# Kernel optimization log

Hardware: AMD Instinct MI355X
Metric: run time of the kernel (lower is better)

## Reference

```python
import jax, jax.numpy as jnp
import numpy as np

# Module constants (match init_kwargs)
M = 2049                      # NpointsMesh (odd)
TAU = 2.821e-5                # Gaussian spreading width ~ 12*(pi/M)^2
XLIMS = (0.0, 10.0)
L = abs(XLIMS[1] - XLIMS[0])
KGRID = jnp.asarray(np.linspace(-(M // 2), M // 2, M), dtype=jnp.float32)        # (M,)
XGRID = jnp.asarray(2.0 * np.pi * np.linspace(XLIMS[0], XLIMS[1], M + 1)[:-1] / L,
                    dtype=jnp.float32)                                           # (M,)
FOUR_PI = 4.0 * np.pi


def setup_inputs() -> dict:
    key = jax.random.key(0)
    kx, = jax.random.split(key, 1)
    x = jax.random.uniform(kx, (16, 1024), dtype=jnp.float32) * 10.0  # points in [xLims[0], xLims[1])
    ones = jnp.ones((1,), dtype=jnp.float32)  # tf.initializers.ones for all 4 weights
    return {"x": x, "shift0": ones, "amp0": ones, "shift1": ones, "amp1": ones}


def reference(x, shift0, amp0, shift1, amp1):
    # Gaussian spreading: (B, N, M)
    diff = x[..., None] * (2.0 * np.pi / L) - XGRID
    g = jnp.exp(-jnp.square(diff) / (4.0 * TAU))
    # Sum over points -> gridded density (B, M), then FFT + shift
    gsum = jnp.sum(g, axis=1).astype(jnp.complex64)
    fft_g = jnp.fft.fftshift(jnp.fft.fft(gsum, axis=-1), axes=-1) * (L / (2.0 * np.pi))
    # Deconvolution of the Gaussian kernel (real-valued)
    deconv = jnp.sqrt(np.pi / TAU) * jnp.exp(jnp.square(KGRID) * TAU)  # (M,)
    rfft = fft_g * deconv  # (B, M) complex
    # Fourier multipliers (real; imag parts are structurally zero in the original)
    m1 = -amp0 * FOUR_PI / (jnp.square(KGRID) + jnp.square(5.0 * shift0))            # (M,)
    m2 = amp1 * FOUR_PI * jnp.square(1.0 / (jnp.square(KGRID) + jnp.square(5.0 * shift1)))  # (M,)
    mult = jnp.stack([m1, m2], axis=0)  # (2, M)
    mult_fft = mult[None, :, :].astype(jnp.complex64) * rfft[:, None, :]  # (B, 2, M)
    mult_deconv = mult_fft * deconv  # second deconv application, as in the original
    # Inverse FFT back to the mesh, keep real part: (B, 2, M)
    irfft = jnp.real(jnp.fft.ifft(jnp.fft.ifftshift(mult_deconv, axes=-1), axis=-1))
    # Inverse interpolation back to the points: (B, N, 2, M) -> (B, N, 2)
    local = irfft[:, None, :, :] * g[:, :, None, :]
    fmm = jnp.sum(local, axis=-1) / M
    return fmm
```

## Files before the change

kernel.cpp:

```cpp
#include <hip/hip_runtime.h>
#include <math.h>

#define M_   2049
#define B_   16
#define N_   1024
#define TAU_ 2.821e-5
#define PI_  3.14159265358979323846
#define TWO_PI_ 6.283185307179586476925286766559

#define CV_SPLIT 16
#define MPAD     2052

#define GS_CH    8
#define HT_BLKS  65
#define FMM_LPP  16

#define SW(i) ((i) + ((i) >> 2))

__global__ __launch_bounds__(256)
void spread_h4(const float* __restrict__ x,
               const float* __restrict__ s0, const float* __restrict__ a0,
               const float* __restrict__ s1, const float* __restrict__ a1,
               double* __restrict__ gsum_part, double* __restrict__ hhalf) {
    __shared__ double smem[4803];
    const int bx  = blockIdx.x;
    const int tid = threadIdx.x;

    if (bx < GS_CH * B_) {
        const int b  = bx >> 3;
        const int ch = bx & (GS_CH - 1);
        for (int i = tid; i < M_; i += 256) smem[i] = 0.0;
        __syncthreads();
        const int pl  = tid >> 1;
        const int sub = tid & 1;
        const double du      = TWO_PI_ / (double)M_;
        const double inv4tau = 1.0 / (4.0 * TAU_);
        const double xv = (double)x[(b << 10) + (ch << 7) + pl];
        const double u  = xv * (TWO_PI_ / 10.0);
        const int mc = (int)(xv * ((double)M_ / 10.0) + 0.5);
        const int start = mc - 33 + sub * 34;
        for (int i = 0; i < 34; ++i) {
            int m = start + i;
            if (m >= 0 && m < M_) {
                double d = u - du * (double)m;
                double t = d * d * inv4tau;
                if (t < 88.0) atomicAdd(&smem[m], (double)__expf(-(float)t));
            }
        }
        __syncthreads();
        double* gp = gsum_part + ((size_t)ch * B_ + b) * M_;
        for (int i = tid; i < M_; i += 256) gp[i] = smem[i];
    } else {
        const int dtile = bx - GS_CH * B_;
        double* costab = smem;
        double* cf0    = smem + 2049;
        double* cf1    = smem + 3073;
        double* red    = smem + 4097;
        double* cc     = smem + 4609;
        double* cs     = smem + 4642;
        double* fc     = smem + 4675;
        double* fs     = smem + 4739;
        const double th = TWO_PI_ / (double)M_;
        if (tid < 33) {
            double a = th * 64.0 * (double)tid;
            cc[tid] = cos(a);
            cs[tid] = sin(a);
        } else if (tid >= 64 && tid < 128) {
            double a = th * (double)(tid - 64);
            fc[tid - 64] = cos(a);
            fs[tid - 64] = sin(a);
        }
        const double sA = 5.0 * (double)s0[0], sB = 5.0 * (double)s1[0];
        const double amp0 = (double)a0[0],     amp1 = (double)a1[0];
        for (int jj = tid; jj < 1024; jj += 256) {
            double j  = (double)(jj + 1);
            double k2 = j * j;
            double dec2 = (PI_ / TAU_) * exp(2.0 * TAU_ * k2);
            double base = 2.0 * (10.0 / TWO_PI_) * dec2 / (double)M_;
            cf0[jj] = base * (-amp0 * 4.0 * PI_ / (k2 + sA * sA));
            double den = k2 + sB * sB;
            cf1[jj] = base * (amp1 * 4.0 * PI_ / (den * den));
        }
        __syncthreads();
        for (int i = tid; i < M_; i += 256) {
            int q = i >> 6, r = i & 63;
            costab[i] = cc[q] * fc[r] - cs[q] * fs[r];
        }
        __syncthreads();
        const int dl = tid & 15;
        const int jq = tid >> 4;
        const int d  = (dtile << 4) + dl;
        double acc0 = 0.0, acc1 = 0.0;
        if (d <= 1024) {
            const int jlo = (jq << 6) + 1;
            int r = (int)(((long long)jlo * (long long)d) % M_);
            #pragma unroll 4
            for (int jj = 0; jj < 64; ++jj) {
                double cv_ = costab[r];
                acc0 += cf0[(jq << 6) + jj] * cv_;
                acc1 += cf1[(jq << 6) + jj] * cv_;
                r += d; if (r >= M_) r -= M_;
            }
        }
        red[tid]       = acc0;
        red[256 + tid] = acc1;
        __syncthreads();
        if (tid < 16) {
            const int dd = (dtile << 4) + tid;
            if (dd <= 1024) {
                const double w0base = (10.0 / TWO_PI_) * (PI_ / TAU_) / (double)M_;
                double h0 = w0base * (-amp0 * 4.0 * PI_ / (sA * sA));
                double h1 = w0base * (amp1 * 4.0 * PI_ / ((sB * sB) * (sB * sB)));
                #pragma unroll
                for (int q = 0; q < 16; ++q) {
                    h0 += red[(q << 4) + tid];
                    h1 += red[256 + (q << 4) + tid];
                }
                hhalf[dd]        = h0;
                hhalf[1025 + dd] = h1;
            }
        }
    }
}

__global__ void conv_kernel(const double* __restrict__ gsum_part,
                            const double* __restrict__ hhalf,
                            double* __restrict__ part) {
    __shared__ double w0s[1456];
    __shared__ double w1s[1456];
    __shared__ double red[512];
    __shared__ double gls[132];
    const int mt = blockIdx.x;
    const int s  = blockIdx.y;
    const int b  = blockIdx.z;
    const int m0  = mt * 1024;
    const int p0  = (s * M_) / CV_SPLIT;
    const int p1  = ((s + 1) * M_) / CV_SPLIT;
    const int len = p1 - p0;
    const int wcount = 1024 + len;
    int base = m0 - (p0 + len - 1);
    while (base < 0) base += M_;
    for (int i = threadIdx.x; i < wcount; i += 256) {
        int idx = base + i;
        while (idx >= M_) idx -= M_;
        int dd = (idx > 1024) ? (M_ - idx) : idx;
        w0s[SW(i)] = hhalf[dd];
        w1s[SW(i)] = hhalf[1025 + dd];
    }
    for (int i = threadIdx.x; i < len; i += 256) {
        double acc = 0.0;
        #pragma unroll
        for (int ch = 0; ch < GS_CH; ++ch)
            acc += gsum_part[((size_t)ch * B_ + b) * M_ + p0 + i];
        gls[i] = acc;
    }
    __syncthreads();

    const int q = 4 * threadIdx.x + len - 1;
    double A0 = w0s[SW(q)], A1 = w0s[SW(q+1)], A2 = w0s[SW(q+2)], A3 = w0s[SW(q+3)];
    double C0 = w1s[SW(q)], C1 = w1s[SW(q+1)], C2 = w1s[SW(q+2)], C3 = w1s[SW(q+3)];
    double a00=0.0,a01=0.0,a02=0.0,a03=0.0, a10=0.0,a11=0.0,a12=0.0,a13=0.0;
    int j = q, tt = 0;
    for (; tt + 4 <= len; tt += 4) {
        double g;
        g = gls[tt];
        a00 += g*A0; a01 += g*A1; a02 += g*A2; a03 += g*A3;
        a10 += g*C0; a11 += g*C1; a12 += g*C2; a13 += g*C3;
        A3 = w0s[SW(j-1)]; C3 = w1s[SW(j-1)];
        g = gls[tt+1];
        a00 += g*A3; a01 += g*A0; a02 += g*A1; a03 += g*A2;
        a10 += g*C3; a11 += g*C0; a12 += g*C1; a13 += g*C2;
        A2 = w0s[SW(j-2)]; C2 = w1s[SW(j-2)];
        g = gls[tt+2];
        a00 += g*A2; a01 += g*A3; a02 += g*A0; a03 += g*A1;
        a10 += g*C2; a11 += g*C3; a12 += g*C0; a13 += g*C1;
        A1 = w0s[SW(j-3)]; C1 = w1s[SW(j-3)];
        g = gls[tt+3];
        a00 += g*A1; a01 += g*A2; a02 += g*A3; a03 += g*A0;
        a10 += g*C1; a11 += g*C2; a12 += g*C3; a13 += g*C0;
        A0 = w0s[SW(j-4)]; C0 = w1s[SW(j-4)];
        j -= 4;
    }
    for (; tt < len; ++tt) {
        double g = gls[tt];
        a00 += g*A0; a01 += g*A1; a02 += g*A2; a03 += g*A3;
        a10 += g*C0; a11 += g*C1; a12 += g*C2; a13 += g*C3;
    }
    {
        double* pv = part + (((size_t)s * B_ + b) * 2) * MPAD + m0 + 4 * threadIdx.x;
        pv[0]        = a00; pv[1]        = a01; pv[2]        = a02; pv[3]        = a03;
        pv[MPAD + 0] = a10; pv[MPAD + 1] = a11; pv[MPAD + 2] = a12; pv[MPAD + 3] = a13;
    }
    if (mt == 1) {
        double t0 = 0.0, t1 = 0.0;
        if (threadIdx.x < len) {
            double g = gls[threadIdx.x];
            int qq = 1023 + len - threadIdx.x;
            t0 = g * w0s[SW(qq)];
            t1 = g * w1s[SW(qq)];
        }
        red[threadIdx.x]       = t0;
        red[256 + threadIdx.x] = t1;
        __syncthreads();
        for (int off = 128; off > 0; off >>= 1) {
            if (threadIdx.x < off) {
                red[threadIdx.x]       += red[threadIdx.x + off];
                red[256 + threadIdx.x] += red[256 + threadIdx.x + off];
            }
            __syncthreads();
        }
        if (threadIdx.x == 0) {
            double* pv = part + (((size_t)s * B_ + b) * 2) * MPAD;
            pv[2048]        = red[0];
            pv[MPAD + 2048] = red[256];
        }
    }
}

__global__ void reduce_kernel(const double* __restrict__ part, double* __restrict__ conv) {
    const int idx = blockIdx.x * 256 + threadIdx.x;
    if (idx >= B_ * 2 * M_) return;
    const int b  = idx / (2 * M_);
    const int rm = idx - b * 2 * M_;
    const int c  = rm / M_;
    const int m  = rm - c * M_;
    const size_t off = ((size_t)b * 2 + c) * MPAD + m;
    const size_t sstride = (size_t)B_ * 2 * MPAD;
    double acc = 0.0;
    #pragma unroll
    for (int k = 0; k < CV_SPLIT; ++k)
        acc += part[(size_t)k * sstride + off];
    conv[idx] = acc;
}

__global__ void fmm_kernel(const float* __restrict__ x, const double* __restrict__ conv,
                           float* __restrict__ out) {
    const int gid = blockIdx.x * 256 + threadIdx.x;
    const int pt  = gid / FMM_LPP;
    const int sub = gid % FMM_LPP;
    const int b   = pt >> 10;
    const double du      = TWO_PI_ / (double)M_;
    const double inv4tau = 1.0 / (4.0 * TAU_);
    const double xv = (double)x[pt];
    const double u  = xv * (TWO_PI_ / 10.0);
    int mc = (int)(xv * ((double)M_ / 10.0) + 0.5);
    int lo = mc - 34; if (lo < 0) lo = 0;
    int hi = mc + 34; if (hi > M_ - 1) hi = M_ - 1;
    const double* c0 = conv + (size_t)(b * 2) * M_;
    const double* c1 = c0 + M_;
    double a0 = 0.0, a1 = 0.0;
    for (int m = lo + sub; m <= hi; m += FMM_LPP) {
        double d = u - du * (double)m;
        double g = (double)__expf(-(float)(d * d * inv4tau));
        a0 += g * c0[m];
        a1 += g * c1[m];
    }
    a0 += __shfl_xor(a0, 1); a1 += __shfl_xor(a1, 1);
    a0 += __shfl_xor(a0, 2); a1 += __shfl_xor(a1, 2);
    a0 += __shfl_xor(a0, 4); a1 += __shfl_xor(a1, 4);
    a0 += __shfl_xor(a0, 8); a1 += __shfl_xor(a1, 8);
    if (sub == 0) {
        out[pt * 2 + 0] = (float)(a0 / (double)M_);
        out[pt * 2 + 1] = (float)(a1 / (double)M_);
    }
}

extern "C" void kernel_launch(void* const* d_in, const int* in_sizes, int n_in,
                              void* d_out, int out_size, void* d_ws, size_t ws_size,
                              hipStream_t stream) {
    (void)in_sizes; (void)n_in; (void)out_size; (void)ws_size;
    const float* x  = (const float*)d_in[0];
    const float* s0 = (const float*)d_in[1];
    const float* a0 = (const float*)d_in[2];
    const float* s1 = (const float*)d_in[3];
    const float* a1 = (const float*)d_in[4];
    float* out = (float*)d_out;

    double* gsum_part = (double*)d_ws;
    double* hhalf     = gsum_part + GS_CH * B_ * M_;
    double* conv      = hhalf + 2 * 1025;
    double* part      = conv + B_ * 2 * M_;

    hipLaunchKernelGGL(spread_h4, dim3(GS_CH * B_ + HT_BLKS), dim3(256), 0, stream,
                       x, s0, a0, s1, a1, gsum_part, hhalf);
    hipLaunchKernelGGL(conv_kernel, dim3(2, CV_SPLIT, B_), dim3(256), 0, stream,
                       gsum_part, hhalf, part);
    hipLaunchKernelGGL(reduce_kernel, dim3((B_ * 2 * M_ + 255) / 256), dim3(256), 0, stream,
                       part, conv);
    hipLaunchKernelGGL(fmm_kernel, dim3(B_ * N_ * FMM_LPP / 256), dim3(256), 0, stream,
                       x, conv, out);
}
```

Measured before the change: 89.40 us.

## Retile circular convolution into smaller output tiles and pre-reduce gsum partials

Moves the summation of the per-chunk gsum partials out of the convolution kernel into its own small kernel, so each conv block reads one precomputed density row instead of re-summing eight partials. The convolution is retiled from 2 output tiles of 1024 with 16 input splits to 4 tiles of 512 with 8 splits, and each thread now produces 2 outputs instead of 4. Together these change the block count, per-thread register tiling and shared-memory footprint, aiming for better occupancy and less redundant global reads. The cost is an extra kernel launch and fewer outputs per thread, so each shared-memory weight load is reused across fewer accumulations.

```diff
diff --git a/kernel.cpp b/kernel.cpp
--- a/kernel.cpp
+++ b/kernel.cpp
@@ -8,7 +8,9 @@
 #define PI_  3.14159265358979323846
 #define TWO_PI_ 6.283185307179586476925286766559
 
-#define CV_SPLIT 16
+#define CV_SPLIT 8
+#define MT_TILES 4
+#define MEXT     512
 #define MPAD     2052
 
 #define GS_CH    8
@@ -123,21 +125,32 @@
     }
 }
 
-__global__ void conv_kernel(const double* __restrict__ gsum_part,
-                            const double* __restrict__ hhalf,
-                            double* __restrict__ part) {
-    __shared__ double w0s[1456];
-    __shared__ double w1s[1456];
+__global__ void gsum_reduce(const double* __restrict__ gsum_part,
+                            double* __restrict__ gsum) {
+    const int idx = blockIdx.x * 256 + threadIdx.x;
+    if (idx >= B_ * M_) return;
+    double acc = 0.0;
+    #pragma unroll
+    for (int ch = 0; ch < GS_CH; ++ch)
+        acc += gsum_part[(size_t)ch * B_ * M_ + idx];
+    gsum[idx] = acc;
+}
+
+__global__ __launch_bounds__(256)
+void conv_kernel(const double* __restrict__ gsum, const double* __restrict__ hhalf,
+                 double* __restrict__ part) {
+    __shared__ double w0s[968];
+    __shared__ double w1s[968];
     __shared__ double red[512];
-    __shared__ double gls[132];
+    __shared__ double gls[260];
     const int mt = blockIdx.x;
     const int s  = blockIdx.y;
     const int b  = blockIdx.z;
-    const int m0  = mt * 1024;
+    const int m0  = mt * MEXT;
     const int p0  = (s * M_) / CV_SPLIT;
     const int p1  = ((s + 1) * M_) / CV_SPLIT;
     const int len = p1 - p0;
-    const int wcount = 1024 + len;
+    const int wcount = MEXT + len;
     int base = m0 - (p0 + len - 1);
     while (base < 0) base += M_;
     for (int i = threadIdx.x; i < wcount; i += 256) {
@@ -147,57 +160,44 @@
         w0s[SW(i)] = hhalf[dd];
         w1s[SW(i)] = hhalf[1025 + dd];
     }
-    for (int i = threadIdx.x; i < len; i += 256) {
-        double acc = 0.0;
-        #pragma unroll
-        for (int ch = 0; ch < GS_CH; ++ch)
-            acc += gsum_part[((size_t)ch * B_ + b) * M_ + p0 + i];
-        gls[i] = acc;
-    }
+    for (int i = threadIdx.x; i < len; i += 256)
+        gls[i] = gsum[(size_t)b * M_ + p0 + i];
     __syncthreads();
 
-    const int q = 4 * threadIdx.x + len - 1;
-    double A0 = w0s[SW(q)], A1 = w0s[SW(q+1)], A2 = w0s[SW(q+2)], A3 = w0s[SW(q+3)];
-    double C0 = w1s[SW(q)], C1 = w1s[SW(q+1)], C2 = w1s[SW(q+2)], C3 = w1s[SW(q+3)];
-    double a00=0.0,a01=0.0,a02=0.0,a03=0.0, a10=0.0,a11=0.0,a12=0.0,a13=0.0;
+    const int q = 2 * threadIdx.x + len - 1;
+    double A0 = w0s[SW(q)], A1 = w0s[SW(q+1)];
+    double C0 = w1s[SW(q)], C1 = w1s[SW(q+1)];
+    double a00 = 0.0, a01 = 0.0, a10 = 0.0, a11 = 0.0;
     int j = q, tt = 0;
-    for (; tt + 4 <= len; tt += 4) {
+    for (; tt + 2 <= len; tt += 2) {
         double g;
         g = gls[tt];
-        a00 += g*A0; a01 += g*A1; a02 += g*A2; a03 += g*A3;
-        a10 += g*C0; a11 += g*C1; a12 += g*C2; a13 += g*C3;
-        A3 = w0s[SW(j-1)]; C3 = w1s[SW(j-1)];
+        a00 += g * A0; a01 += g * A1;
+        a10 += g * C0; a11 += g * C1;
+        A1 = w0s[SW(j-1)]; C1 = w1s[SW(j-1)];
         g = gls[tt+1];
-        a00 += g*A3; a01 += g*A0; a02 += g*A1; a03 += g*A2;
-        a10 += g*C3; a11 += g*C0; a12 += g*C1; a13 += g*C2;
-        A2 = w0s[SW(j-2)]; C2 = w1s[SW(j-2)];
-        g = gls[tt+2];
-        a00 += g*A2; a01 += g*A3; a02 += g*A0; a03 += g*A1;
-        a10 += g*C2; a11 += g*C3; a12 += g*C0; a13 += g*C1;
-        A1 = w0s[SW(j-3)]; C1 = w1s[SW(j-3)];
-        g = gls[tt+3];
-        a00 += g*A1; a01 += g*A2; a02 += g*A3; a03 += g*A0;
-        a10 += g*C1; a11 += g*C2; a12 += g*C3; a13 += g*C0;
-        A0 = w0s[SW(j-4)]; C0 = w1s[SW(j-4)];
-        j -= 4;
-    }
-    for (; tt < len; ++tt) {
+        a00 += g * A1; a01 += g * A0;
+        a10 += g * C1; a11 += g * C0;
+        A0 = w0s[SW(j-2)]; C0 = w1s[SW(j-2)];
+        j -= 2;
+    }
+    if (tt < len) {
         double g = gls[tt];
-        a00 += g*A0; a01 += g*A1; a02 += g*A2; a03 += g*A3;
-        a10 += g*C0; a11 += g*C1; a12 += g*C2; a13 += g*C3;
+        a00 += g * A0; a01 += g * A1;
+        a10 += g * C0; a11 += g * C1;
     }
     {
-        double* pv = part + (((size_t)s * B_ + b) * 2) * MPAD + m0 + 4 * threadIdx.x;
-        pv[0]        = a00; pv[1]        = a01; pv[2]        = a02; pv[3]        = a03;
-        pv[MPAD + 0] = a10; pv[MPAD + 1] = a11; pv[MPAD + 2] = a12; pv[MPAD + 3] = a13;
-    }
-    if (mt == 1) {
+        double* pv = part + (((size_t)s * B_ + b) * 2) * MPAD + m0 + 2 * threadIdx.x;
+        pv[0]        = a00; pv[1]        = a01;
+        pv[MPAD + 0] = a10; pv[MPAD + 1] = a11;
+    }
+    if (mt == MT_TILES - 1) {
         double t0 = 0.0, t1 = 0.0;
-        if (threadIdx.x < len) {
-            double g = gls[threadIdx.x];
-            int qq = 1023 + len - threadIdx.x;
-            t0 = g * w0s[SW(qq)];
-            t1 = g * w1s[SW(qq)];
+        for (int t = threadIdx.x; t < len; t += 256) {
+            double g = gls[t];
+            int qq = MEXT + len - 1 - t;
+            t0 += g * w0s[SW(qq)];
+            t1 += g * w1s[SW(qq)];
         }
         red[threadIdx.x]       = t0;
         red[256 + threadIdx.x] = t1;
@@ -277,14 +277,17 @@
     float* out = (float*)d_out;
 
     double* gsum_part = (double*)d_ws;
-    double* hhalf     = gsum_part + GS_CH * B_ * M_;
+    double* gsum      = gsum_part + GS_CH * B_ * M_;
+    double* hhalf     = gsum + B_ * M_;
     double* conv      = hhalf + 2 * 1025;
     double* part      = conv + B_ * 2 * M_;
 
     hipLaunchKernelGGL(spread_h4, dim3(GS_CH * B_ + HT_BLKS), dim3(256), 0, stream,
                        x, s0, a0, s1, a1, gsum_part, hhalf);
-    hipLaunchKernelGGL(conv_kernel, dim3(2, CV_SPLIT, B_), dim3(256), 0, stream,
-                       gsum_part, hhalf, part);
+    hipLaunchKernelGGL(gsum_reduce, dim3((B_ * M_ + 255) / 256), dim3(256), 0, stream,
+                       gsum_part, gsum);
+    hipLaunchKernelGGL(conv_kernel, dim3(MT_TILES, CV_SPLIT, B_), dim3(256), 0, stream,
+                       gsum, hhalf, part);
     hipLaunchKernelGGL(reduce_kernel, dim3((B_ * 2 * M_ + 255) / 256), dim3(256), 0, stream,
                        part, conv);
     hipLaunchKernelGGL(fmm_kernel, dim3(B_ * N_ * FMM_LPP / 256), dim3(256), 0, stream,
```

Result: slower. 93.95 us (+5.1%).
